# Performance work log

Measured on AMD Instinct MI355X. Metric: run time of the kernel, lower is better.

Reference implementation:

```python
import jax, jax.numpy as jnp
import numpy as np

N, IN_DIM, OUT_DIM = 2048, 128, 64
ALPHA = 0.2  # LeakyReLU negative slope


def setup_inputs() -> dict:
    key = jax.random.key(0)
    k1, k2, k3 = jax.random.split(key, 3)
    H = jax.random.normal(k1, (N, IN_DIM), dtype=jnp.float32)
    # Xavier-uniform-like init for W [out_dim, in_dim] (torch Linear weight layout)
    limit_w = float(np.sqrt(6.0 / (IN_DIM + OUT_DIM)))
    W = jax.random.uniform(k2, (OUT_DIM, IN_DIM), dtype=jnp.float32,
                           minval=-limit_w, maxval=limit_w)
    limit_a = float(np.sqrt(6.0 / (OUT_DIM + 1)))
    a = jax.random.uniform(k3, (OUT_DIM,), dtype=jnp.float32,
                           minval=-limit_a, maxval=limit_a)
    return {"H": H, "W": W, "a": a}


def reference(H, W, a):
    # Wh: [N, D]
    Wh = H @ W.T
    # e[i, j] = leakyrelu(Wh[i] + Wh[j]) . a   -> [N, N]
    e = jnp.einsum('ijd,d->ij',
                   jax.nn.leaky_relu(Wh[:, None, :] + Wh[None, :, :],
                                     negative_slope=ALPHA),
                   a)
    attention = jax.nn.softmax(e, axis=1)  # softmax over j (columns)
    return attention @ Wh  # [N, D]
```

## Files before the change

kernel.cpp:

```cpp
#include <hip/hip_runtime.h>
#include <hip/hip_fp16.h>

#define N 2048
#define IN_DIM 128
#define D 64
#define ALPHA 0.2f
#define TI 4
#define BLK 512
#define NW (BLK / 64)


typedef _Float16 half2v __attribute__((ext_vector_type(2)));

__device__ __forceinline__ unsigned short f2h_rne(float f) {
  return __half_as_ushort(__float2half(f));
}

__device__ __forceinline__ float dot2abs(unsigned s2, unsigned w2,
                                         unsigned a2, float acc) {
  half2v sv = __builtin_bit_cast(half2v, s2);
  half2v wv = __builtin_bit_cast(half2v, w2);
  half2v t = sv + wv;
  unsigned tu = __builtin_bit_cast(unsigned, t) & 0x7fff7fffu;
  return __builtin_amdgcn_fdot2(__builtin_bit_cast(half2v, tu),
                                __builtin_bit_cast(half2v, a2),
                                acc, false);
}

__device__ __forceinline__ float dot2u(unsigned p2, unsigned w2, float acc) {
  return __builtin_amdgcn_fdot2(__builtin_bit_cast(half2v, p2),
                                __builtin_bit_cast(half2v, w2),
                                acc, false);
}

__device__ __forceinline__ unsigned cvt_pk_u(float lo, float hi) {
  return __builtin_bit_cast(unsigned, __builtin_amdgcn_cvt_pkrtz(lo, hi));
}

__global__ __launch_bounds__(256) void wh_kernel(
    const float* __restrict__ H, const float* __restrict__ W,
    const float* __restrict__ a, unsigned short* __restrict__ Whh,
    unsigned int* __restrict__ WhP, unsigned int* __restrict__ WhQ,
    float* __restrict__ bs2, unsigned int* __restrict__ ap2) {
  __shared__ float wlds[D][IN_DIM + 1];
  __shared__ float hl[8 * IN_DIM];
  const int t = threadIdx.x;
  const int i0 = blockIdx.x * 8;

  if (blockIdx.x == 0 && t < D / 2) {
    ap2[t] = (unsigned)f2h_rne(0.4f * a[2 * t]) |
             ((unsigned)f2h_rne(0.4f * a[2 * t + 1]) << 16);
  }

  #pragma unroll
  for (int rep = 0; rep < 8; ++rep) {
    int idx = rep * 1024 + t * 4;
    float4 w4 = *(const float4*)&W[idx];
    int d = idx / IN_DIM, k = idx % IN_DIM;
    wlds[d][k] = w4.x; wlds[d][k + 1] = w4.y;
    wlds[d][k + 2] = w4.z; wlds[d][k + 3] = w4.w;
  }
  *(float4*)&hl[t * 4] = *(const float4*)&H[i0 * IN_DIM + t * 4];
  __syncthreads();

  const int wid = t >> 6, lane = t & 63;
  const float av = a[lane];
  const int lr0 = wid * 2, lr1 = lr0 + 1;
  const int ia = i0 + lr0, ib = i0 + lr1;

  float acc0 = 0.f, acc1 = 0.f;
  #pragma unroll 4
  for (int k = 0; k < IN_DIM; ++k) {
    float wv = wlds[lane][k];
    acc0 = fmaf(hl[lr0 * IN_DIM + k], wv, acc0);
    acc1 = fmaf(hl[lr1 * IN_DIM + k], wv, acc1);
  }

  unsigned h0 = f2h_rne(acc0), h1 = f2h_rne(acc1);
  Whh[ia * D + lane] = (unsigned short)h0;
  Whh[ib * D + lane] = (unsigned short)h1;
  unsigned q0 = (unsigned)__shfl_xor((int)h0, 1);
  unsigned q1 = (unsigned)__shfl_xor((int)h1, 1);
  if (!(lane & 1)) {
    WhP[(lane >> 1) * N + ia] = h0 | (q0 << 16);
    WhP[(lane >> 1) * N + ib] = h1 | (q1 << 16);
  }
  WhQ[(blockIdx.x * 4 + wid) * D + lane] = h0 | (h1 << 16);

  float pb0 = av * acc0, pb1 = av * acc1;
  #pragma unroll
  for (int off = 32; off; off >>= 1) {
    pb0 += __shfl_xor(pb0, off);
    pb1 += __shfl_xor(pb1, off);
  }
  const float L2E = 1.4426950408889634f;
  if (lane == 0) {
    bs2[ia] = fmaf(0.6f * pb0, L2E, -6.f);
    bs2[ib] = fmaf(0.6f * pb1, L2E, -6.f);
  }
}

__global__ __launch_bounds__(BLK, 4) void attn_kernel(
    const unsigned short* __restrict__ Whh,
    const unsigned int* __restrict__ WhP,
    const unsigned int* __restrict__ WhQ,
    const float* __restrict__ bs2, const unsigned int* __restrict__ ap2,
    float* __restrict__ out) {
  __shared__ unsigned short p_lds[TI][N];
  __shared__ float red2s[TI][NW];
  __shared__ float part[NW][TI][D];
  __shared__ uint4 stage[TI * 8 + D / 8];

  const int t = threadIdx.x;
  const int i0 = blockIdx.x * TI;
  const int wid = t >> 6, lane = t & 63;

  if (t < TI * 8 + D / 8) {
    stage[t] = (t < TI * 8) ? ((const uint4*)(Whh + i0 * D))[t]
                            : ((const uint4*)ap2)[t - TI * 8];
  }
  __syncthreads();

  const int j0 = t * 4;
  float4 bj = *(const float4*)&bs2[j0];
  float4 ac[TI];
  #pragma unroll
  for (int ti = 0; ti < TI; ++ti) { ac[ti].x = ac[ti].y = ac[ti].z = ac[ti].w = 0.f; }

  const unsigned int* wp = WhP + j0;

  uint4 wbuf[2][4], sbuf[2][TI], abuf[2];
  #pragma unroll
  for (int q = 0; q < 4; ++q) wbuf[0][q] = *(const uint4*)&wp[q * N];
  #pragma unroll
  for (int ti = 0; ti < TI; ++ti) sbuf[0][ti] = stage[ti * 8];
  abuf[0] = stage[TI * 8];

  #pragma unroll
  for (int c = 0; c < D / 8; ++c) {
    const int cur = c & 1, nxt = cur ^ 1;
    if (c < D / 8 - 1) {
      #pragma unroll
      for (int q = 0; q < 4; ++q)
        wbuf[nxt][q] = *(const uint4*)&wp[((c + 1) * 4 + q) * N];
      #pragma unroll
      for (int ti = 0; ti < TI; ++ti) sbuf[nxt][ti] = stage[ti * 8 + c + 1];
      abuf[nxt] = stage[TI * 8 + c + 1];
    }
    #pragma unroll
    for (int q = 0; q < 4; ++q) {
      const unsigned a2 = (q == 0) ? abuf[cur].x : (q == 1) ? abuf[cur].y
                        : (q == 2) ? abuf[cur].z : abuf[cur].w;
      const uint4 w4 = wbuf[cur][q];
      #pragma unroll
      for (int ti = 0; ti < TI; ++ti) {
        const unsigned s2 = (q == 0) ? sbuf[cur][ti].x : (q == 1) ? sbuf[cur][ti].y
                          : (q == 2) ? sbuf[cur][ti].z : sbuf[cur][ti].w;
        ac[ti].x = dot2abs(s2, w4.x, a2, ac[ti].x);
        ac[ti].y = dot2abs(s2, w4.y, a2, ac[ti].y);
        ac[ti].z = dot2abs(s2, w4.z, a2, ac[ti].z);
        ac[ti].w = dot2abs(s2, w4.w, a2, ac[ti].w);
      }
    }
  }

  const float L2E = 1.4426950408889634f;
  float s_t[TI];
  #pragma unroll
  for (int ti = 0; ti < TI; ++ti) {
    float4 p4;
    p4.x = __builtin_amdgcn_exp2f(fmaf(ac[ti].x, L2E, bj.x));
    p4.y = __builtin_amdgcn_exp2f(fmaf(ac[ti].y, L2E, bj.y));
    p4.z = __builtin_amdgcn_exp2f(fmaf(ac[ti].z, L2E, bj.z));
    p4.w = __builtin_amdgcn_exp2f(fmaf(ac[ti].w, L2E, bj.w));
    uint2 ph;
    ph.x = cvt_pk_u(p4.x, p4.y);
    ph.y = cvt_pk_u(p4.z, p4.w);
    *(uint2*)&p_lds[ti][j0] = ph;
    s_t[ti] = (p4.x + p4.y) + (p4.z + p4.w);
  }
  #pragma unroll
  for (int off = 32; off; off >>= 1) {
    #pragma unroll
    for (int ti = 0; ti < TI; ++ti)
      s_t[ti] += __shfl_xor(s_t[ti], off);
  }
  if (lane == 0) {
    #pragma unroll
    for (int ti = 0; ti < TI; ++ti) red2s[ti][wid] = s_t[ti];
  }
  __syncthreads();

  const int jbase = wid * (N / NW);
  const int hi4 = (lane >> 4) * 4;
  const int col = (lane & 15) * 4;
  float4 acc[TI];
  #pragma unroll
  for (int ti = 0; ti < TI; ++ti) { acc[ti].x = acc[ti].y = acc[ti].z = acc[ti].w = 0.f; }

  uint4 wq[2][2];
  uint2 pt[2][TI];
  {
    const int r0 = jbase + hi4;
    wq[0][0] = *(const uint4*)&WhQ[(r0 >> 1) * D + col];
    wq[0][1] = *(const uint4*)&WhQ[((r0 >> 1) + 1) * D + col];
    #pragma unroll
    for (int ti = 0; ti < TI; ++ti)
      pt[0][ti] = *(const uint2*)&p_lds[ti][r0];
  }

  #pragma unroll
  for (int it = 0; it < (N / NW) / 16; ++it) {
    const int cur = it & 1, nxt = cur ^ 1;
    if (it < (N / NW) / 16 - 1) {
      const int r1 = jbase + (it + 1) * 16 + hi4;
      wq[nxt][0] = *(const uint4*)&WhQ[(r1 >> 1) * D + col];
      wq[nxt][1] = *(const uint4*)&WhQ[((r1 >> 1) + 1) * D + col];
      #pragma unroll
      for (int ti = 0; ti < TI; ++ti)
        pt[nxt][ti] = *(const uint2*)&p_lds[ti][r1];
    }
    #pragma unroll
    for (int ti = 0; ti < TI; ++ti) {
      const unsigned ppA = pt[cur][ti].x;
      const unsigned ppB = pt[cur][ti].y;
      acc[ti].x = dot2u(ppB, wq[cur][1].x, dot2u(ppA, wq[cur][0].x, acc[ti].x));
      acc[ti].y = dot2u(ppB, wq[cur][1].y, dot2u(ppA, wq[cur][0].y, acc[ti].y));
      acc[ti].z = dot2u(ppB, wq[cur][1].z, dot2u(ppA, wq[cur][0].z, acc[ti].z));
      acc[ti].w = dot2u(ppB, wq[cur][1].w, dot2u(ppA, wq[cur][0].w, acc[ti].w));
    }
  }
  #pragma unroll
  for (int ti = 0; ti < TI; ++ti) {
    acc[ti].x += __shfl_xor(acc[ti].x, 16);
    acc[ti].y += __shfl_xor(acc[ti].y, 16);
    acc[ti].z += __shfl_xor(acc[ti].z, 16);
    acc[ti].w += __shfl_xor(acc[ti].w, 16);
    acc[ti].x += __shfl_xor(acc[ti].x, 32);
    acc[ti].y += __shfl_xor(acc[ti].y, 32);
    acc[ti].z += __shfl_xor(acc[ti].z, 32);
    acc[ti].w += __shfl_xor(acc[ti].w, 32);
  }
  if (lane < 16) {
    #pragma unroll
    for (int ti = 0; ti < TI; ++ti)
      *(float4*)&part[wid][ti][lane * 4] = acc[ti];
  }
  __syncthreads();
  if (t < TI * D) {
    const int ti = t >> 6, dd = t & 63;
    float s = 0.f;
    #pragma unroll
    for (int w = 0; w < NW; ++w) s += part[w][ti][dd];
    float4 r0 = *(const float4*)&red2s[ti][0];
    float4 r1 = *(const float4*)&red2s[ti][4];
    float rsum = ((r0.x + r0.y) + (r0.z + r0.w)) +
                 ((r1.x + r1.y) + (r1.z + r1.w));
    out[(i0 + ti) * D + dd] = s * (1.f / rsum);
  }
}

extern "C" void kernel_launch(void* const* d_in, const int* in_sizes, int n_in,
                              void* d_out, int out_size, void* d_ws, size_t ws_size,
                              hipStream_t stream) {
  const float* H = (const float*)d_in[0];
  const float* W = (const float*)d_in[1];
  const float* a = (const float*)d_in[2];
  float* out = (float*)d_out;

  unsigned short* Whh = (unsigned short*)d_ws;
  unsigned int* WhP = (unsigned int*)(Whh + N * D);
  unsigned int* WhQ = WhP + (D / 2) * N;
  float* bs2 = (float*)(WhQ + (N / 2) * D);
  unsigned int* ap2 = (unsigned int*)(bs2 + N);

  wh_kernel<<<N / 8, 256, 0, stream>>>(H, W, a, Whh, WhP, WhQ, bs2, ap2);
  attn_kernel<<<N / TI, BLK, 0, stream>>>(Whh, WhP, WhQ, bs2, ap2, out);
}
```

Baseline: 30.27 us.

## Process 8 rows per block with 1024 threads, 2 columns per thread

Doubles rows per block (TI 4→8) and threads per block (512→1024), so each thread now scores 2 columns instead of 4 against 8 query rows. Each WhP column load is reused across twice as many rows, which halves global traffic per output row, and the grid shrinks to 256 blocks. The LDS-staged register double-buffering of row and attention vectors is replaced by direct per-iteration LDS reads, and the final reduction loops over 16 waves. LDS use roughly doubles, and fewer blocks may leave the device underoccupied.

```diff
diff --git a/kernel.cpp b/kernel.cpp
--- a/kernel.cpp
+++ b/kernel.cpp
@@ -5,8 +5,8 @@
 #define IN_DIM 128
 #define D 64
 #define ALPHA 0.2f
-#define TI 4
-#define BLK 512
+#define TI 8
+#define BLK 1024
 #define NW (BLK / 64)
 
 
@@ -121,20 +121,17 @@
   }
   __syncthreads();
 
-  const int j0 = t * 4;
-  float4 bj = *(const float4*)&bs2[j0];
-  float4 ac[TI];
-  #pragma unroll
-  for (int ti = 0; ti < TI; ++ti) { ac[ti].x = ac[ti].y = ac[ti].z = ac[ti].w = 0.f; }
+  const int j0 = t * 2;
+  float2 bj = *(const float2*)&bs2[j0];
+  float2 ac[TI];
+  #pragma unroll
+  for (int ti = 0; ti < TI; ++ti) { ac[ti].x = ac[ti].y = 0.f; }
 
   const unsigned int* wp = WhP + j0;
 
-  uint4 wbuf[2][4], sbuf[2][TI], abuf[2];
-  #pragma unroll
-  for (int q = 0; q < 4; ++q) wbuf[0][q] = *(const uint4*)&wp[q * N];
-  #pragma unroll
-  for (int ti = 0; ti < TI; ++ti) sbuf[0][ti] = stage[ti * 8];
-  abuf[0] = stage[TI * 8];
+  uint2 wbuf[2][4];
+  #pragma unroll
+  for (int q = 0; q < 4; ++q) wbuf[0][q] = *(const uint2*)&wp[q * N];
 
   #pragma unroll
   for (int c = 0; c < D / 8; ++c) {
@@ -142,24 +139,23 @@
     if (c < D / 8 - 1) {
       #pragma unroll
       for (int q = 0; q < 4; ++q)
-        wbuf[nxt][q] = *(const uint4*)&wp[((c + 1) * 4 + q) * N];
-      #pragma unroll
-      for (int ti = 0; ti < TI; ++ti) sbuf[nxt][ti] = stage[ti * 8 + c + 1];
-      abuf[nxt] = stage[TI * 8 + c + 1];
-    }
+        wbuf[nxt][q] = *(const uint2*)&wp[((c + 1) * 4 + q) * N];
+    }
+    const uint4 a4 = stage[TI * 8 + c];
+    uint4 s4l[TI];
+    #pragma unroll
+    for (int ti = 0; ti < TI; ++ti) s4l[ti] = stage[ti * 8 + c];
     #pragma unroll
     for (int q = 0; q < 4; ++q) {
-      const unsigned a2 = (q == 0) ? abuf[cur].x : (q == 1) ? abuf[cur].y
-                        : (q == 2) ? abuf[cur].z : abuf[cur].w;
-      const uint4 w4 = wbuf[cur][q];
+      const unsigned a2 = (q == 0) ? a4.x : (q == 1) ? a4.y
+                        : (q == 2) ? a4.z : a4.w;
+      const uint2 w2 = wbuf[cur][q];
       #pragma unroll
       for (int ti = 0; ti < TI; ++ti) {
-        const unsigned s2 = (q == 0) ? sbuf[cur][ti].x : (q == 1) ? sbuf[cur][ti].y
-                          : (q == 2) ? sbuf[cur][ti].z : sbuf[cur][ti].w;
-        ac[ti].x = dot2abs(s2, w4.x, a2, ac[ti].x);
-        ac[ti].y = dot2abs(s2, w4.y, a2, ac[ti].y);
-        ac[ti].z = dot2abs(s2, w4.z, a2, ac[ti].z);
-        ac[ti].w = dot2abs(s2, w4.w, a2, ac[ti].w);
+        const unsigned s2 = (q == 0) ? s4l[ti].x : (q == 1) ? s4l[ti].y
+                          : (q == 2) ? s4l[ti].z : s4l[ti].w;
+        ac[ti].x = dot2abs(s2, w2.x, a2, ac[ti].x);
+        ac[ti].y = dot2abs(s2, w2.y, a2, ac[ti].y);
       }
     }
   }
@@ -168,16 +164,10 @@
   float s_t[TI];
   #pragma unroll
   for (int ti = 0; ti < TI; ++ti) {
-    float4 p4;
-    p4.x = __builtin_amdgcn_exp2f(fmaf(ac[ti].x, L2E, bj.x));
-    p4.y = __builtin_amdgcn_exp2f(fmaf(ac[ti].y, L2E, bj.y));
-    p4.z = __builtin_amdgcn_exp2f(fmaf(ac[ti].z, L2E, bj.z));
-    p4.w = __builtin_amdgcn_exp2f(fmaf(ac[ti].w, L2E, bj.w));
-    uint2 ph;
-    ph.x = cvt_pk_u(p4.x, p4.y);
-    ph.y = cvt_pk_u(p4.z, p4.w);
-    *(uint2*)&p_lds[ti][j0] = ph;
-    s_t[ti] = (p4.x + p4.y) + (p4.z + p4.w);
+    float px = __builtin_amdgcn_exp2f(fmaf(ac[ti].x, L2E, bj.x));
+    float py = __builtin_amdgcn_exp2f(fmaf(ac[ti].y, L2E, bj.y));
+    *(unsigned*)&p_lds[ti][j0] = cvt_pk_u(px, py);
+    s_t[ti] = px + py;
   }
   #pragma unroll
   for (int off = 32; off; off >>= 1) {
@@ -252,10 +242,12 @@
     float s = 0.f;
     #pragma unroll
     for (int w = 0; w < NW; ++w) s += part[w][ti][dd];
-    float4 r0 = *(const float4*)&red2s[ti][0];
-    float4 r1 = *(const float4*)&red2s[ti][4];
-    float rsum = ((r0.x + r0.y) + (r0.z + r0.w)) +
-                 ((r1.x + r1.y) + (r1.z + r1.w));
+    float rsum = 0.f;
+    #pragma unroll
+    for (int w = 0; w < NW; w += 4) {
+      float4 r = *(const float4*)&red2s[ti][w];
+      rsum += ((r.x + r.y) + (r.z + r.w));
+    }
     out[(i0 + ti) * D + dd] = s * (1.f / rsum);
   }
 }
```

Result: slower. 33.22 us (+9.8%).

## Split wh_kernel K-reduction across threads and hoist WhQ prefetch earlier

Applied to the files above, without the earlier changes.

The projection kernel now uses 512-thread blocks over 4 rows, splitting each dot product's K dimension in two halves that are reduced through shared memory. This doubles the block count and shortens each thread's serial FMA chain, at the cost of extra syncs and reloading W per block. The WhQ packing goes through LDS. In the attention kernel the first WhQ global prefetch is moved ahead of the exp/softmax stage to hide its latency.

```diff
diff --git a/kernel.cpp b/kernel.cpp
--- a/kernel.cpp
+++ b/kernel.cpp
@@ -37,15 +37,18 @@
   return __builtin_bit_cast(unsigned, __builtin_amdgcn_cvt_pkrtz(lo, hi));
 }
 
-__global__ __launch_bounds__(256) void wh_kernel(
+__global__ __launch_bounds__(512) void wh_kernel(
     const float* __restrict__ H, const float* __restrict__ W,
     const float* __restrict__ a, unsigned short* __restrict__ Whh,
     unsigned int* __restrict__ WhP, unsigned int* __restrict__ WhQ,
     float* __restrict__ bs2, unsigned int* __restrict__ ap2) {
   __shared__ float wlds[D][IN_DIM + 1];
-  __shared__ float hl[8 * IN_DIM];
+  __shared__ float hl[4 * IN_DIM];
+  __shared__ float partial[512];
+  __shared__ __align__(16) unsigned short hh[4][D];
   const int t = threadIdx.x;
-  const int i0 = blockIdx.x * 8;
+  const int i0 = blockIdx.x * 4;
+  const float L2E = 1.4426950408889634f;
 
   if (blockIdx.x == 0 && t < D / 2) {
     ap2[t] = (unsigned)f2h_rne(0.4f * a[2 * t]) |
@@ -53,50 +56,46 @@
   }
 
   #pragma unroll
-  for (int rep = 0; rep < 8; ++rep) {
-    int idx = rep * 1024 + t * 4;
+  for (int rep = 0; rep < 4; ++rep) {
+    int idx = (rep * 512 + t) * 4;
     float4 w4 = *(const float4*)&W[idx];
-    int d = idx / IN_DIM, k = idx % IN_DIM;
+    int d = idx >> 7, k = idx & 127;
     wlds[d][k] = w4.x; wlds[d][k + 1] = w4.y;
     wlds[d][k + 2] = w4.z; wlds[d][k + 3] = w4.w;
   }
-  *(float4*)&hl[t * 4] = *(const float4*)&H[i0 * IN_DIM + t * 4];
-  __syncthreads();
-
-  const int wid = t >> 6, lane = t & 63;
-  const float av = a[lane];
-  const int lr0 = wid * 2, lr1 = lr0 + 1;
-  const int ia = i0 + lr0, ib = i0 + lr1;
-
-  float acc0 = 0.f, acc1 = 0.f;
-  #pragma unroll 4
-  for (int k = 0; k < IN_DIM; ++k) {
-    float wv = wlds[lane][k];
-    acc0 = fmaf(hl[lr0 * IN_DIM + k], wv, acc0);
-    acc1 = fmaf(hl[lr1 * IN_DIM + k], wv, acc1);
-  }
-
-  unsigned h0 = f2h_rne(acc0), h1 = f2h_rne(acc1);
-  Whh[ia * D + lane] = (unsigned short)h0;
-  Whh[ib * D + lane] = (unsigned short)h1;
-  unsigned q0 = (unsigned)__shfl_xor((int)h0, 1);
-  unsigned q1 = (unsigned)__shfl_xor((int)h1, 1);
-  if (!(lane & 1)) {
-    WhP[(lane >> 1) * N + ia] = h0 | (q0 << 16);
-    WhP[(lane >> 1) * N + ib] = h1 | (q1 << 16);
-  }
-  WhQ[(blockIdx.x * 4 + wid) * D + lane] = h0 | (h1 << 16);
-
-  float pb0 = av * acc0, pb1 = av * acc1;
-  #pragma unroll
-  for (int off = 32; off; off >>= 1) {
-    pb0 += __shfl_xor(pb0, off);
-    pb1 += __shfl_xor(pb1, off);
-  }
-  const float L2E = 1.4426950408889634f;
-  if (lane == 0) {
-    bs2[ia] = fmaf(0.6f * pb0, L2E, -6.f);
-    bs2[ib] = fmaf(0.6f * pb1, L2E, -6.f);
+  if (t < 128)
+    *(float4*)&hl[t * 4] = *(const float4*)&H[i0 * IN_DIM + t * 4];
+  __syncthreads();
+
+  {
+    const int oi = t & 255, kh = t >> 8;
+    const int r = oi >> 6, d = oi & 63;
+    float acc = 0.f;
+    #pragma unroll 8
+    for (int k = 0; k < 64; ++k)
+      acc = fmaf(hl[r * IN_DIM + kh * 64 + k], wlds[d][kh * 64 + k], acc);
+    partial[t] = acc;
+  }
+  __syncthreads();
+
+  if (t < 256) {
+    const int r = t >> 6, d = t & 63;
+    const float acc = partial[t] + partial[t + 256];
+    const unsigned myh = f2h_rne(acc);
+    hh[r][d] = (unsigned short)myh;
+    Whh[(i0 + r) * D + d] = (unsigned short)myh;
+    const unsigned hq = (unsigned)__shfl_xor((int)myh, 1);
+    if (!(d & 1)) WhP[(d >> 1) * N + (i0 + r)] = myh | (hq << 16);
+    float pb = a[d] * acc;
+    #pragma unroll
+    for (int off = 32; off; off >>= 1) pb += __shfl_xor(pb, off);
+    if (d == 0) bs2[i0 + r] = fmaf(0.6f * pb, L2E, -6.f);
+  }
+  __syncthreads();
+  if (t < 128) {
+    const int pr = t >> 6, d = t & 63;
+    const unsigned lo = hh[pr * 2][d], hi = hh[pr * 2 + 1][d];
+    WhQ[((i0 >> 1) + pr) * D + d] = lo | (hi << 16);
   }
 }
 
@@ -162,6 +161,16 @@
         ac[ti].w = dot2abs(s2, w4.w, a2, ac[ti].w);
       }
     }
+  }
+
+  const int jbase = wid * (N / NW);
+  const int hi4 = (lane >> 4) * 4;
+  const int col = (lane & 15) * 4;
+  uint4 wq[2][2];
+  {
+    const int r0 = jbase + hi4;
+    wq[0][0] = *(const uint4*)&WhQ[(r0 >> 1) * D + col];
+    wq[0][1] = *(const uint4*)&WhQ[((r0 >> 1) + 1) * D + col];
   }
 
   const float L2E = 1.4426950408889634f;
@@ -191,19 +200,13 @@
   }
   __syncthreads();
 
-  const int jbase = wid * (N / NW);
-  const int hi4 = (lane >> 4) * 4;
-  const int col = (lane & 15) * 4;
   float4 acc[TI];
   #pragma unroll
   for (int ti = 0; ti < TI; ++ti) { acc[ti].x = acc[ti].y = acc[ti].z = acc[ti].w = 0.f; }
 
-  uint4 wq[2][2];
   uint2 pt[2][TI];
   {
     const int r0 = jbase + hi4;
-    wq[0][0] = *(const uint4*)&WhQ[(r0 >> 1) * D + col];
-    wq[0][1] = *(const uint4*)&WhQ[((r0 >> 1) + 1) * D + col];
     #pragma unroll
     for (int ti = 0; ti < TI; ++ti)
       pt[0][ti] = *(const uint2*)&p_lds[ti][r0];
@@ -274,6 +277,6 @@
   float* bs2 = (float*)(WhQ + (N / 2) * D);
   unsigned int* ap2 = (unsigned int*)(bs2 + N);
 
-  wh_kernel<<<N / 8, 256, 0, stream>>>(H, W, a, Whh, WhP, WhQ, bs2, ap2);
+  wh_kernel<<<N / 4, 512, 0, stream>>>(H, W, a, Whh, WhP, WhQ, bs2, ap2);
   attn_kernel<<<N / TI, BLK, 0, stream>>>(Whh, WhP, WhQ, bs2, ap2, out);
 }
```

After: 29.68 us. Within noise of the previous version (-1.9%).
